# Kernel tuning notes

Hardware: AMD Instinct MI355X
Metric: run time of the kernel (lower is better)

The kernel has to match this reference:

```python
import jax, jax.numpy as jnp
import numpy as np

N, E, D, H = 50000, 800000, 128, 8
C = D // H  # head dim = 16

def _layer_norm(x, g, b, eps=1e-5):
    mu = jnp.mean(x, axis=-1, keepdims=True)
    var = jnp.var(x, axis=-1, keepdims=True)
    return (x - mu) * jax.lax.rsqrt(var + eps) * g + b

def setup_inputs() -> dict:
    key = jax.random.key(0)
    ks = jax.random.split(key, 24)
    def lin(i, fan_in=D):
        s = 1.0 / np.sqrt(fan_in)
        return (jax.random.uniform(ks[i], (D, D), minval=-s, maxval=s),
                jax.random.uniform(ks[i + 1], (D,), minval=-s, maxval=s))
    Wq, bq = lin(0); Wk, bk = lin(2); Wv, bv = lin(4)
    We, be = lin(6); Ws, bs = lin(8)
    W1, b1 = lin(10); W2, b2 = lin(12)
    return {
        'edge_index': jax.random.randint(ks[14], (2, E), 0, N),
        'node_attr': jax.random.normal(ks[15], (N, D), dtype=jnp.float32),
        'edge_attr': jax.random.normal(ks[16], (E, D), dtype=jnp.float32),
        'Wq': Wq, 'bq': bq, 'Wk': Wk, 'bk': bk, 'Wv': Wv, 'bv': bv,
        'We': We, 'be': be, 'Ws': Ws, 'bs': bs,
        'W1': W1, 'b1': b1, 'W2': W2, 'b2': b2,
        'ln1_g': jnp.ones((D,)), 'ln1_b': jnp.zeros((D,)),
        'ln2_g': jnp.ones((D,)), 'ln2_b': jnp.zeros((D,)),
    }

def _transformer_conv(node_attr, edge_attr, src, dst, Wq, bq, Wk, bk, Wv, bv, We, be, Ws, bs):
    # PyG TransformerConv, concat=True, root_weight=True, beta=False, eval (no dropout)
    q = (node_attr @ Wq.T + bq).reshape(N, H, C)[dst]          # [E,H,C]
    e = (edge_attr @ We.T + be).reshape(E, H, C)               # [E,H,C]
    k = (node_attr @ Wk.T + bk).reshape(N, H, C)[src] + e      # [E,H,C]
    v = (node_attr @ Wv.T + bv).reshape(N, H, C)[src] + e      # [E,H,C]
    alpha = jnp.sum(q * k, axis=-1) / jnp.sqrt(jnp.float32(C)) # [E,H]
    # segment softmax over destination node
    m = jax.ops.segment_max(alpha, dst, num_segments=N)        # [N,H]
    ex = jnp.exp(alpha - m[dst])
    denom = jax.ops.segment_sum(ex, dst, num_segments=N)       # [N,H]
    a = ex / (denom[dst] + 1e-16)                              # [E,H]
    out = jax.ops.segment_sum(v * a[..., None], dst, num_segments=N)  # [N,H,C]
    out = out.reshape(N, D)
    return out + node_attr @ Ws.T + bs  # root/skip connection

def reference(edge_index, node_attr, edge_attr, Wq, bq, Wk, bk, Wv, bv, We, be,
              Ws, bs, W1, b1, W2, b2, ln1_g, ln1_b, ln2_g, ln2_b):
    src, dst = edge_index[0], edge_index[1]
    x = _transformer_conv(node_attr, edge_attr, src, dst,
                          Wq, bq, Wk, bk, Wv, bv, We, be, Ws, bs)
    node_attr = node_attr + _layer_norm(x, ln1_g, ln1_b)
    h = jax.nn.silu(node_attr @ W1.T + b1) @ W2.T + b2
    node_attr = node_attr + _layer_norm(h, ln2_g, ln2_b)
    return node_attr
```

## Files before the change

### kernel.cpp

```cpp
#include <hip/hip_runtime.h>
#include <hip/hip_fp16.h>

#define N_NODES 50000
#define N_EDGES 800000
#define DIM 128
#define NODE_TILES 782
#define EDGE_TILES 12500
#define SCAN_NB 50

typedef _Float16 f16;
typedef _Float16 f16x2 __attribute__((ext_vector_type(2)));
typedef _Float16 f16x4 __attribute__((ext_vector_type(4)));
typedef _Float16 f16x8 __attribute__((ext_vector_type(8)));
typedef float    f32x16 __attribute__((ext_vector_type(16)));

__device__ __forceinline__ void sfence() { __builtin_amdgcn_sched_barrier(0); }

__device__ __forceinline__ void load_wfrag(const f16* __restrict__ Wh, int ch, int l31, int g,
                                           f16x8 bf[2][8]) {
#pragma unroll
  for (int c = 0; c < 2; ++c)
#pragma unroll
    for (int ks = 0; ks < 8; ++ks)
      bf[c][ks] = *(const f16x8*)(Wh + ((ch * 64 + c * 32 + l31) << 7) + 16 * ks + 8 * g);
}

__device__ __forceinline__ void stage_issue(const float* __restrict__ X, long M, long base,
                                            int tid, float4 sv[8]) {
#pragma unroll
  for (int kk = 0; kk < 8; ++kk) {
    int i = tid + kk * 256;
    long row = base + (i >> 5);
    long gr = row < M ? row : (M - 1);
    sv[kk] = *(const float4*)(X + gr * DIM + (i & 31) * 4);
  }
}

__device__ __forceinline__ void stage_write(const float4 sv[8], int tid, f16* __restrict__ lds) {
#pragma unroll
  for (int kk = 0; kk < 8; ++kk) {
    int i = tid + kk * 256;
    int r = i >> 5, s8 = i & 31;
    f16x4 h;
    h[0] = (f16)sv[kk].x; h[1] = (f16)sv[kk].y; h[2] = (f16)sv[kk].z; h[3] = (f16)sv[kk].w;
    *(f16x4*)(lds + r * 128 + (((s8 >> 1) ^ (r & 15)) << 3) + ((s8 & 1) << 2)) = h;
  }
}

__device__ __forceinline__ void mfma_lds_g(const f16* __restrict__ A, int lr, int g,
                                           const f16x8 bf[2][8], f32x16 acc[2]) {
#pragma unroll
  for (int c = 0; c < 2; ++c)
#pragma unroll
    for (int k = 0; k < 16; ++k) acc[c][k] = 0.0f;
#pragma unroll
  for (int ks = 0; ks < 8; ++ks) {
    f16x8 a = *(const f16x8*)(A + lr * 128 + (((2 * ks + g) ^ (lr & 15)) << 3));
    acc[0] = __builtin_amdgcn_mfma_f32_32x32x16_f16(a, bf[0][ks], acc[0], 0, 0, 0);
    acc[1] = __builtin_amdgcn_mfma_f32_32x32x16_f16(a, bf[1][ks], acc[1], 0, 0, 0);
  }
}

__device__ __forceinline__ void load_wfrag1(const f16* __restrict__ Wh, int cc, int l31, int g,
                                            f16x8 bf[8]) {
#pragma unroll
  for (int ks = 0; ks < 8; ++ks)
    bf[ks] = *(const f16x8*)(Wh + ((cc * 32 + l31) << 7) + 16 * ks + 8 * g);
}

__device__ __forceinline__ void stage_issue512(const float* __restrict__ X, long M, long base,
                                               int tid, float4 sv[4]) {
#pragma unroll
  for (int kk = 0; kk < 4; ++kk) {
    int i = tid + kk * 512;
    long row = base + (i >> 5);
    long gr = row < M ? row : (M - 1);
    sv[kk] = *(const float4*)(X + gr * DIM + (i & 31) * 4);
  }
}

__device__ __forceinline__ void stage_write512(const float4 sv[4], int tid,
                                               f16* __restrict__ lds) {
#pragma unroll
  for (int kk = 0; kk < 4; ++kk) {
    int i = tid + kk * 512;
    int r = i >> 5, s8 = i & 31;
    f16x4 h;
    h[0] = (f16)sv[kk].x; h[1] = (f16)sv[kk].y; h[2] = (f16)sv[kk].z; h[3] = (f16)sv[kk].w;
    *(f16x4*)(lds + r * 128 + (((s8 >> 1) ^ (r & 15)) << 3) + ((s8 & 1) << 2)) = h;
  }
}

__device__ __forceinline__ void mfma1(const f16* __restrict__ A, int lr, int g,
                                      const f16x8 bf[8], f32x16& acc) {
#pragma unroll
  for (int k = 0; k < 16; ++k) acc[k] = 0.0f;
#pragma unroll
  for (int ks = 0; ks < 8; ++ks) {
    f16x8 a = *(const f16x8*)(A + lr * 128 + (((2 * ks + g) ^ (lr & 15)) << 3));
    acc = __builtin_amdgcn_mfma_f32_32x32x16_f16(a, bf[ks], acc, 0, 0, 0);
  }
}

template <int HALF_OUT>
__device__ __forceinline__ void gemm_store1(const f32x16& acc, long M,
                                            const float* __restrict__ Bv,
                                            void* __restrict__ OUT,
                                            long tile0, int rc, int cc, int l31, int g) {
  int col = cc * 32 + l31;
  float bv = Bv[col];
#pragma unroll
  for (int r = 0; r < 16; ++r) {
    long gm = tile0 + rc * 32 + ((r & 3) + 8 * (r >> 2) + 4 * g);
    if (gm < M) {
      float v = acc[r] + bv;
      if (HALF_OUT) ((f16*)OUT)[gm * DIM + col] = (f16)v;
      else          ((float*)OUT)[gm * DIM + col] = v;
    }
  }
}

__global__ __launch_bounds__(512, 4) void big_gemms(const float* __restrict__ X,
    const float* __restrict__ EA,
    const f16* __restrict__ WhAll,
    const float* __restrict__ bq, const float* __restrict__ bk,
    const float* __restrict__ bv_, const float* __restrict__ bs, const float* __restrict__ be,
    f16* __restrict__ Q, f16* __restrict__ K, f16* __restrict__ V, float* __restrict__ S,
    f16* __restrict__ emat) {
  __shared__ f16 lbuf[64 * 128];
  int tid = threadIdx.x;
  int lane = tid & 63, w = tid >> 6;
  int rc = w >> 2, cc = w & 3, l31 = lane & 31, g = lane >> 5;
  int lr = rc * 32 + l31;

  if (blockIdx.x < NODE_TILES) {
    long tile0 = (long)blockIdx.x * 64;
    float4 sv[4];
    stage_issue512(X, N_NODES, tile0, tid, sv);
    stage_write512(sv, tid, lbuf);
    __syncthreads();
#pragma unroll 1
    for (int mat = 0; mat < 4; ++mat) {
      f16x8 bf[8];
      load_wfrag1(WhAll + mat * 16384, cc, l31, g, bf);
      f32x16 acc;
      mfma1(lbuf, lr, g, bf, acc);
      if (mat == 0)      gemm_store1<1>(acc, N_NODES, bq, Q, tile0, rc, cc, l31, g);
      else if (mat == 1) gemm_store1<1>(acc, N_NODES, bk, K, tile0, rc, cc, l31, g);
      else if (mat == 2) gemm_store1<1>(acc, N_NODES, bv_, V, tile0, rc, cc, l31, g);
      else               gemm_store1<0>(acc, N_NODES, bs, S, tile0, rc, cc, l31, g);
    }
    return;
  }

  long tile0 = (long)(blockIdx.x - NODE_TILES) * 64;
  float4 sv[4];
  stage_issue512(EA, (long)N_EDGES, tile0, tid, sv);
  stage_write512(sv, tid, lbuf);
  __syncthreads();
  f16x8 bf[8];
  load_wfrag1(WhAll + 4 * 16384, cc, l31, g, bf);
  f32x16 acc;
  mfma1(lbuf, lr, g, bf, acc);
  gemm_store1<1>(acc, (long)N_EDGES, be, emat, tile0, rc, cc, l31, g);
}

__global__ __launch_bounds__(256) void mlp_ln(const float* __restrict__ X,
    const f16* __restrict__ W1h, const float* __restrict__ b1,
    const f16* __restrict__ W2h, const float* __restrict__ b2,
    const float* __restrict__ gv, const float* __restrict__ bv,
    float* __restrict__ outp) {
  __shared__ float smem[64 * 128];
  f16* xs = (f16*)smem;
  f16* hs = (f16*)smem + 64 * 128;
  float* wbuf = smem;
  int tid = threadIdx.x;
  int lane = tid & 63, w = tid >> 6;
  int rc = w >> 1, ch = w & 1, l31 = lane & 31, g = lane >> 5;
  int t = blockIdx.x;
  if (t >= NODE_TILES) return;
  long tile0 = (long)t * 64;
  int lr = rc * 32 + l31;

  float4 sv[8];
  stage_issue(X, N_NODES, tile0, tid, sv);
  f16x8 bf1[2][8];
  load_wfrag(W1h, ch, l31, g, bf1);
  stage_write(sv, tid, xs);
  __syncthreads();

  f32x16 acc[2];
  mfma_lds_g(xs, lr, g, bf1, acc);
  f16x8 bf2[2][8];
  load_wfrag(W2h, ch, l31, g, bf2);

#pragma unroll
  for (int c = 0; c < 2; ++c) {
    int col = ch * 64 + c * 32 + l31;
    float bb = b1[col];
#pragma unroll
    for (int r = 0; r < 16; ++r) {
      int row = rc * 32 + (r & 3) + 8 * (r >> 2) + 4 * g;
      float v = acc[c][r] + bb;
      v = v / (1.0f + __expf(-v));
      hs[row * 128 + (((col >> 3) ^ (row & 15)) << 3) + (col & 7)] = (f16)v;
    }
  }
  __syncthreads();

  f32x16 a2[2];
  mfma_lds_g(hs, lr, g, bf2, a2);
  __syncthreads();

#pragma unroll
  for (int c = 0; c < 2; ++c) {
    int col = ch * 64 + c * 32 + l31;
    float bb = b2[col];
#pragma unroll
    for (int r = 0; r < 16; ++r) {
      int row = rc * 32 + (r & 3) + 8 * (r >> 2) + 4 * g;
      wbuf[row * 128 + col] = a2[c][r] + bb;
    }
  }
  __syncthreads();

  float2 gg = *(const float2*)(gv + 2 * lane);
  float2 bb2 = *(const float2*)(bv + 2 * lane);
#pragma unroll 1
  for (int rr = 0; rr < 16; ++rr) {
    int row = w * 16 + rr;
    long gm = tile0 + row;
    if (gm >= N_NODES) break;
    float2 x;
    x.x = wbuf[row * 128 + 2 * lane];
    x.y = wbuf[row * 128 + 2 * lane + 1];
    float sm = x.x + x.y;
    for (int m = 1; m < 64; m <<= 1) sm += __shfl_xor(sm, m);
    float mu = sm * (1.f / 128.f);
    float dx = x.x - mu, dy = x.y - mu;
    float ss = dx * dx + dy * dy;
    for (int m = 1; m < 64; m <<= 1) ss += __shfl_xor(ss, m);
    float r = rsqrtf(ss * (1.f / 128.f) + 1e-5f);
    float2 bs = *(const float2*)(X + gm * DIM + 2 * lane);
    float2 o;
    o.x = bs.x + dx * r * gg.x + bb2.x;
    o.y = bs.y + dy * r * gg.y + bb2.y;
    *(float2*)(outp + gm * DIM + 2 * lane) = o;
  }
}

__global__ void hist_conv_k(const int* __restrict__ ei, int* __restrict__ counts,
                            const float* __restrict__ a0, const float* __restrict__ a1,
                            const float* __restrict__ a2, const float* __restrict__ a3,
                            const float* __restrict__ a4, const float* __restrict__ a5,
                            const float* __restrict__ a6, f16* __restrict__ dst) {
  long gid = blockIdx.x * 256L + threadIdx.x;
  if (gid < 7 * 16384) {
    int mat = (int)(gid >> 14), el = (int)(gid & 16383);
    const float* s = (mat == 0) ? a0 : (mat == 1) ? a1 : (mat == 2) ? a2 : (mat == 3) ? a3
                   : (mat == 4) ? a4 : (mat == 5) ? a5 : a6;
    dst[gid] = (f16)s[el];
  }
  for (long e = gid; e < N_EDGES; e += 1024L * 256)
    atomicAdd(&counts[ei[N_EDGES + e]], 1);
}

__global__ __launch_bounds__(1024) void blocksum_k(const int* __restrict__ counts,
                                                   int* __restrict__ bsum) {
  __shared__ int sd[1024];
  int t = threadIdx.x, b = blockIdx.x;
  int v = (t < 1000) ? counts[b * 1000 + t] : 0;
  sd[t] = v; __syncthreads();
  for (int off = 512; off > 0; off >>= 1) {
    if (t < off) sd[t] += sd[t + off];
    __syncthreads();
  }
  if (t == 0) bsum[b] = sd[0];
}

__global__ void scan_small(const int* __restrict__ bsum, int* __restrict__ boff,
                           int* __restrict__ offs) {
  if (threadIdx.x == 0) {
    int run = 0;
    for (int b = 0; b < SCAN_NB; ++b) { boff[b] = run; run += bsum[b]; }
    boff[SCAN_NB] = run;
    offs[N_NODES] = run;
  }
}

__global__ __launch_bounds__(1024) void expand_k(const int* __restrict__ counts,
                                                 const int* __restrict__ boff,
                                                 int* __restrict__ offs, int* __restrict__ cursor) {
  __shared__ int sd[1024];
  int t = threadIdx.x, b = blockIdx.x;
  int v = (t < 1000) ? counts[b * 1000 + t] : 0;
  sd[t] = v; __syncthreads();
  for (int off = 1; off < 1024; off <<= 1) {
    int x = (t >= off) ? sd[t - off] : 0;
    __syncthreads();
    sd[t] += x;
    __syncthreads();
  }
  if (t < 1000) {
    int o = boff[b] + sd[t] - v;
    int idx = b * 1000 + t;
    offs[idx] = o;
    cursor[idx] = o;
  }
}

__global__ void scatter_k(const int* __restrict__ ei, int* __restrict__ cursor,
                          int2* __restrict__ meta) {
  for (long e = blockIdx.x * (long)blockDim.x + threadIdx.x; e < N_EDGES;
       e += (long)gridDim.x * blockDim.x) {
    int d = ei[N_EDGES + e];
    int pos = atomicAdd(&cursor[d], 1);
    meta[pos] = make_int2(ei[e], (int)e);
  }
}

__global__ __launch_bounds__(256) void attn_ln(const int* __restrict__ offs,
    const int2* __restrict__ meta, const f16* __restrict__ emat, const f16* __restrict__ Qn,
    const f16* __restrict__ Kn, const f16* __restrict__ Vn,
    const float* __restrict__ Skip, const float* __restrict__ base,
    const float* __restrict__ gv, const float* __restrict__ bv,
    float* __restrict__ outp) {
  int n = blockIdx.x * 4 + (threadIdx.x >> 6);
  if (n >= N_NODES) return;
  int lane = threadIdx.x & 63;
  int grp = lane >> 4, li = lane & 15;
  int c8 = 8 * li;

  float q[8];
  {
    f16x8 qv = *(const f16x8*)(Qn + (long)n * DIM + c8);
#pragma unroll
    for (int k = 0; k < 8; ++k) q[k] = (float)qv[k];
  }

  int rs = offs[n], re = offs[n + 1];
  float a[8];
#pragma unroll
  for (int k = 0; k < 8; ++k) a[k] = 0.f;
  float den = 0.f;

  if (rs < re) {
    int e0 = rs + grp;
    int2 mCur = meta[(e0 < re) ? e0 : (re - 1)];
    for (int i = rs; i < re; i += 4) {
      int ei_ = i + grp;
      bool valid = ei_ < re;
      int s = mCur.x;
      long eid = mCur.y;
      int en = ei_ + 4;
      mCur = meta[(en < re) ? en : (re - 1)];
      f16x8 e8 = *(const f16x8*)(emat + eid * DIM + c8);
      f16x8 k8 = *(const f16x8*)(Kn + (long)s * DIM + c8);
      f16x8 v8 = *(const f16x8*)(Vn + (long)s * DIM + c8);
      float p = 0.f;
#pragma unroll
      for (int k = 0; k < 8; ++k) p += q[k] * ((float)k8[k] + (float)e8[k]);
      p += __shfl_xor(p, 1);
      float ex = valid ? __expf(p * 0.25f) : 0.f;
      den += ex;
#pragma unroll
      for (int k = 0; k < 8; ++k) a[k] += ex * ((float)e8[k] + (float)v8[k]);
    }
  }
#pragma unroll
  for (int k = 0; k < 8; ++k) {
    a[k] += __shfl_xor(a[k], 16);
    a[k] += __shfl_xor(a[k], 32);
  }
  den += __shfl_xor(den, 16);
  den += __shfl_xor(den, 32);

  float inv = 1.f / (den + 1e-16f);
  float x[8];
  {
    float4 sk0 = *(const float4*)(Skip + (long)n * DIM + c8);
    float4 sk1 = *(const float4*)(Skip + (long)n * DIM + c8 + 4);
    x[0] = a[0] * inv + sk0.x; x[1] = a[1] * inv + sk0.y;
    x[2] = a[2] * inv + sk0.z; x[3] = a[3] * inv + sk0.w;
    x[4] = a[4] * inv + sk1.x; x[5] = a[5] * inv + sk1.y;
    x[6] = a[6] * inv + sk1.z; x[7] = a[7] * inv + sk1.w;
  }

  float sm = 0.f;
#pragma unroll
  for (int k = 0; k < 8; ++k) sm += x[k];
  for (int m = 1; m < 16; m <<= 1) sm += __shfl_xor(sm, m);
  float mu = sm * (1.f / 128.f);
  float d[8], ss = 0.f;
#pragma unroll
  for (int k = 0; k < 8; ++k) { d[k] = x[k] - mu; ss += d[k] * d[k]; }
  for (int m = 1; m < 16; m <<= 1) ss += __shfl_xor(ss, m);
  float r = rsqrtf(ss * (1.f / 128.f) + 1e-5f);

  if (grp == 0) {
    float4 g0 = *(const float4*)(gv + c8);
    float4 g1 = *(const float4*)(gv + c8 + 4);
    float4 b0 = *(const float4*)(bv + c8);
    float4 b1 = *(const float4*)(bv + c8 + 4);
    float4 s0 = *(const float4*)(base + (long)n * DIM + c8);
    float4 s1 = *(const float4*)(base + (long)n * DIM + c8 + 4);
    float4 o0, o1;
    o0.x = s0.x + d[0] * r * g0.x + b0.x;
    o0.y = s0.y + d[1] * r * g0.y + b0.y;
    o0.z = s0.z + d[2] * r * g0.z + b0.z;
    o0.w = s0.w + d[3] * r * g0.w + b0.w;
    o1.x = s1.x + d[4] * r * g1.x + b1.x;
    o1.y = s1.y + d[5] * r * g1.y + b1.y;
    o1.z = s1.z + d[6] * r * g1.z + b1.z;
    o1.w = s1.w + d[7] * r * g1.w + b1.w;
    *(float4*)(outp + (long)n * DIM + c8) = o0;
    *(float4*)(outp + (long)n * DIM + c8 + 4) = o1;
  }
}

extern "C" void kernel_launch(void* const* d_in, const int* in_sizes, int n_in,
                              void* d_out, int out_size, void* d_ws, size_t ws_size,
                              hipStream_t stream) {
  (void)in_sizes; (void)n_in; (void)out_size; (void)ws_size;
  const int*   ei  = (const int*)d_in[0];
  const float* x0  = (const float*)d_in[1];
  const float* ea  = (const float*)d_in[2];
  const float* Wq  = (const float*)d_in[3];  const float* bq = (const float*)d_in[4];
  const float* Wk  = (const float*)d_in[5];  const float* bk = (const float*)d_in[6];
  const float* Wv  = (const float*)d_in[7];  const float* bv = (const float*)d_in[8];
  const float* We  = (const float*)d_in[9];  const float* be = (const float*)d_in[10];
  const float* Wsk = (const float*)d_in[11]; const float* bsk = (const float*)d_in[12];
  const float* W1  = (const float*)d_in[13]; const float* b1 = (const float*)d_in[14];
  const float* W2  = (const float*)d_in[15]; const float* b2 = (const float*)d_in[16];
  const float* g1  = (const float*)d_in[17]; const float* lb1 = (const float*)d_in[18];
  const float* g2  = (const float*)d_in[19]; const float* lb2 = (const float*)d_in[20];

  char* ws = (char*)d_ws;
  f16*   Qn     = (f16*)(ws + 0);
  f16*   Kn     = (f16*)(ws + 12800000L);
  f16*   Vn     = (f16*)(ws + 25600000L);
  float* Skip   = (float*)(ws + 38400000L);
  int*   offs   = (int*)(ws + 64000000L);
  int*   cursor = (int*)(ws + 64200192L);
  int*   counts = (int*)(ws + 64429568L);
  int*   bsum   = (int*)(ws + 64629760L);
  int*   boff   = bsum + 64;
  int2*  meta   = (int2*)(ws + 64630272L);
  f16*   emat   = (f16*)(ws + 71030272L);
  float* node1  = (float*)(ws + 275830272L);
  f16*   WhAll  = (f16*)(ws + 301430272L);

  (void)hipMemsetAsync(counts, 0, N_NODES * sizeof(int), stream);
  hist_conv_k<<<1024, 256, 0, stream>>>(ei, counts, Wq, Wk, Wv, Wsk, We, W1, W2, WhAll);
  blocksum_k<<<SCAN_NB, 1024, 0, stream>>>(counts, bsum);
  scan_small<<<1, 64, 0, stream>>>(bsum, boff, offs);
  expand_k<<<SCAN_NB, 1024, 0, stream>>>(counts, boff, offs, cursor);
  scatter_k<<<1024, 256, 0, stream>>>(ei, cursor, meta);

  big_gemms<<<NODE_TILES + EDGE_TILES, 512, 0, stream>>>(
      x0, ea, WhAll, bq, bk, bv, bsk, be, Qn, Kn, Vn, Skip, emat);
  attn_ln<<<12500, 256, 0, stream>>>(offs, meta, emat, Qn, Kn, Vn, Skip, x0, g1, lb1, node1);
  mlp_ln<<<NODE_TILES, 256, 0, stream>>>(node1, WhAll + 5 * 16384, b1,
                                         WhAll + 6 * 16384, b2, g2, lb2, (float*)d_out);
}
```

Measured before the change: 447.7 us.

## Fuse CSR scan into single-pass kernel and overlap edge scatter with GEMMs

Replaces the three-kernel block-sum/scan/expand prefix sum with one decoupled-lookback scan kernel that uses per-block flags and prefixes, zeroed by an enlarged memset. The edge scatter into CSR order is moved into extra blocks appended to the big GEMM grid, so it runs alongside the projection work instead of as a separate launch. This reduces kernel launches and serialization gaps. The cost is a spin-wait chain across scan blocks, which depends on every block being resident.

```diff
diff --git a/kernel.cpp b/kernel.cpp
--- a/kernel.cpp
+++ b/kernel.cpp
@@ -6,6 +6,7 @@
 #define DIM 128
 #define NODE_TILES 782
 #define EDGE_TILES 12500
+#define SCAT_BLKS 1563
 #define SCAN_NB 50
 
 typedef _Float16 f16;
@@ -121,7 +122,8 @@
 }
 
 __global__ __launch_bounds__(512, 4) void big_gemms(const float* __restrict__ X,
-    const float* __restrict__ EA,
+    const float* __restrict__ EA, const int* __restrict__ ei,
+    int* __restrict__ cursor, int2* __restrict__ meta,
     const f16* __restrict__ WhAll,
     const float* __restrict__ bq, const float* __restrict__ bk,
     const float* __restrict__ bv_, const float* __restrict__ bs, const float* __restrict__ be,
@@ -132,6 +134,16 @@
   int lane = tid & 63, w = tid >> 6;
   int rc = w >> 2, cc = w & 3, l31 = lane & 31, g = lane >> 5;
   int lr = rc * 32 + l31;
+
+  if (blockIdx.x >= NODE_TILES + EDGE_TILES) {
+    long e = (long)(blockIdx.x - NODE_TILES - EDGE_TILES) * 512 + tid;
+    if (e < N_EDGES) {
+      int d = ei[N_EDGES + e];
+      int pos = atomicAdd(&cursor[d], 1);
+      meta[pos] = make_int2(ei[e], (int)e);
+    }
+    return;
+  }
 
   if (blockIdx.x < NODE_TILES) {
     long tile0 = (long)blockIdx.x * 64;
@@ -265,57 +277,53 @@
     atomicAdd(&counts[ei[N_EDGES + e]], 1);
 }
 
-__global__ __launch_bounds__(1024) void blocksum_k(const int* __restrict__ counts,
-                                                   int* __restrict__ bsum) {
-  __shared__ int sd[1024];
-  int t = threadIdx.x, b = blockIdx.x;
-  int v = (t < 1000) ? counts[b * 1000 + t] : 0;
-  sd[t] = v; __syncthreads();
-  for (int off = 512; off > 0; off >>= 1) {
-    if (t < off) sd[t] += sd[t + off];
-    __syncthreads();
-  }
-  if (t == 0) bsum[b] = sd[0];
-}
-
-__global__ void scan_small(const int* __restrict__ bsum, int* __restrict__ boff,
-                           int* __restrict__ offs) {
-  if (threadIdx.x == 0) {
-    int run = 0;
-    for (int b = 0; b < SCAN_NB; ++b) { boff[b] = run; run += bsum[b]; }
-    boff[SCAN_NB] = run;
-    offs[N_NODES] = run;
-  }
-}
-
-__global__ __launch_bounds__(1024) void expand_k(const int* __restrict__ counts,
-                                                 const int* __restrict__ boff,
-                                                 int* __restrict__ offs, int* __restrict__ cursor) {
-  __shared__ int sd[1024];
-  int t = threadIdx.x, b = blockIdx.x;
-  int v = (t < 1000) ? counts[b * 1000 + t] : 0;
-  sd[t] = v; __syncthreads();
-  for (int off = 1; off < 1024; off <<= 1) {
+__global__ __launch_bounds__(256) void scan_k2(const int* __restrict__ counts,
+                                               int* __restrict__ offs, int* __restrict__ cursor,
+                                               int* __restrict__ pref, int* __restrict__ flag) {
+  __shared__ int sd[256];
+  __shared__ int carry_s;
+  int b = blockIdx.x, t = threadIdx.x;
+  int base = b * 1000;
+  int v[4];
+  int idx0 = t * 4;
+#pragma unroll
+  for (int k = 0; k < 4; ++k) {
+    int idx = idx0 + k;
+    v[k] = (idx < 1000) ? counts[base + idx] : 0;
+  }
+  int lsum = v[0] + v[1] + v[2] + v[3];
+  sd[t] = lsum;
+  __syncthreads();
+  for (int off = 1; off < 256; off <<= 1) {
     int x = (t >= off) ? sd[t - off] : 0;
     __syncthreads();
     sd[t] += x;
     __syncthreads();
   }
-  if (t < 1000) {
-    int o = boff[b] + sd[t] - v;
-    int idx = b * 1000 + t;
-    offs[idx] = o;
-    cursor[idx] = o;
-  }
-}
-
-__global__ void scatter_k(const int* __restrict__ ei, int* __restrict__ cursor,
-                          int2* __restrict__ meta) {
-  for (long e = blockIdx.x * (long)blockDim.x + threadIdx.x; e < N_EDGES;
-       e += (long)gridDim.x * blockDim.x) {
-    int d = ei[N_EDGES + e];
-    int pos = atomicAdd(&cursor[d], 1);
-    meta[pos] = make_int2(ei[e], (int)e);
+  int texcl = sd[t] - lsum;
+  int bsum = sd[255];
+  if (t == 0) {
+    int c = 0;
+    if (b > 0) {
+      while (atomicAdd(&flag[b - 1], 0) == 0) {}
+      c = atomicAdd(&pref[b - 1], 0);
+    }
+    carry_s = c;
+    atomicExch(&pref[b], c + bsum);
+    __threadfence();
+    atomicExch(&flag[b], 1);
+    if (b == SCAN_NB - 1) offs[N_NODES] = c + bsum;
+  }
+  __syncthreads();
+  int run = carry_s + texcl;
+#pragma unroll
+  for (int k = 0; k < 4; ++k) {
+    int idx = idx0 + k;
+    if (idx < 1000) {
+      offs[base + idx] = run;
+      cursor[base + idx] = run;
+      run += v[k];
+    }
   }
 }
 
@@ -443,22 +451,19 @@
   int*   offs   = (int*)(ws + 64000000L);
   int*   cursor = (int*)(ws + 64200192L);
   int*   counts = (int*)(ws + 64429568L);
-  int*   bsum   = (int*)(ws + 64629760L);
-  int*   boff   = bsum + 64;
+  int*   pref   = (int*)(ws + 64629568L);
+  int*   flag   = (int*)(ws + 64629824L);
   int2*  meta   = (int2*)(ws + 64630272L);
   f16*   emat   = (f16*)(ws + 71030272L);
   float* node1  = (float*)(ws + 275830272L);
   f16*   WhAll  = (f16*)(ws + 301430272L);
 
-  (void)hipMemsetAsync(counts, 0, N_NODES * sizeof(int), stream);
+  (void)hipMemsetAsync(counts, 0, 200704, stream);
   hist_conv_k<<<1024, 256, 0, stream>>>(ei, counts, Wq, Wk, Wv, Wsk, We, W1, W2, WhAll);
-  blocksum_k<<<SCAN_NB, 1024, 0, stream>>>(counts, bsum);
-  scan_small<<<1, 64, 0, stream>>>(bsum, boff, offs);
-  expand_k<<<SCAN_NB, 1024, 0, stream>>>(counts, boff, offs, cursor);
-  scatter_k<<<1024, 256, 0, stream>>>(ei, cursor, meta);
-
-  big_gemms<<<NODE_TILES + EDGE_TILES, 512, 0, stream>>>(
-      x0, ea, WhAll, bq, bk, bv, bsk, be, Qn, Kn, Vn, Skip, emat);
+  scan_k2<<<SCAN_NB, 256, 0, stream>>>(counts, offs, cursor, pref, flag);
+
+  big_gemms<<<NODE_TILES + EDGE_TILES + SCAT_BLKS, 512, 0, stream>>>(
+      x0, ea, ei, cursor, meta, WhAll, bq, bk, bv, bsk, be, Qn, Kn, Vn, Skip, emat);
   attn_ln<<<12500, 256, 0, stream>>>(offs, meta, emat, Qn, Kn, Vn, Skip, x0, g1, lb1, node1);
   mlp_ln<<<NODE_TILES, 256, 0, stream>>>(node1, WhAll + 5 * 16384, b1,
                                          WhAll + 6 * 16384, b2, g2, lb2, (float*)d_out);
```

Result: slower. 498.1 us (+11.3%).
